# Kernel tuning notes

Measured on AMD Instinct MI355X. Metric: run time of the kernel, lower is better.

The kernel has to match this reference:

```python
import jax, jax.numpy as jnp
import numpy as np

LN_EPS = 1e-6


def setup_inputs() -> dict:
    key = jax.random.key(0)
    ks = jax.random.split(key, 8)
    B, C, E, S, K = 2, 32, 128, 64, 7  # E = exp_r * C
    x = jax.random.normal(ks[0], (B, C, S, S, S), jnp.float32)
    mask = (jax.random.uniform(ks[1], (B, 1, S, S, S)) < 0.3).astype(jnp.int32)
    w_dw = jax.random.normal(ks[2], (C, 1, K, K, K), jnp.float32) * 0.05  # depthwise, groups=C
    b_dw = jnp.zeros((C,), jnp.float32)
    ln_g = jnp.ones((C,), jnp.float32)
    ln_b = jnp.zeros((C,), jnp.float32)
    w2 = jax.random.normal(ks[3], (E, C), jnp.float32) * (1.0 / np.sqrt(C))  # 1x1 expand
    b2 = jnp.zeros((E,), jnp.float32)
    w3 = jax.random.normal(ks[4], (C, E), jnp.float32) * (1.0 / np.sqrt(E))  # 1x1 project
    b3 = jnp.zeros((C,), jnp.float32)
    return {"x": x, "mask": mask, "w_dw": w_dw, "b_dw": b_dw,
            "ln_g": ln_g, "ln_b": ln_b, "w2": w2, "b2": b2, "w3": w3, "b3": b3}


def reference(x, mask, w_dw, b_dw, ln_g, ln_b, w2, b2, w3, b3):
    m = mask.astype(x.dtype)                      # [B,1,D,H,W] active-site indicator
    cexp = lambda v: v[None, :, None, None, None]
    xm = x * m                                    # sparse tensor: zeros off the active set
    # submanifold depthwise conv: gather only active neighbors, emit only at active sites
    C = w_dw.shape[0]
    y = jax.lax.conv_general_dilated(
        xm, w_dw, window_strides=(1, 1, 1), padding='SAME',
        feature_group_count=C,
        dimension_numbers=('NCDHW', 'OIDHW', 'NCDHW'))
    y = (y + cexp(b_dw)) * m
    # ConvNeXt LayerNorm: per-voxel over channels, only on active sites
    mu = y.mean(axis=1, keepdims=True)
    var = ((y - mu) ** 2).mean(axis=1, keepdims=True)
    yn = ((y - mu) * jax.lax.rsqrt(var + LN_EPS) * cexp(ln_g) + cexp(ln_b)) * m
    # 1x1 expand + GELU (exact, matching nn.GELU default)
    h = jax.nn.gelu(jnp.einsum('bcdhw,ec->bedhw', yn, w2) + cexp(b2), approximate=False) * m
    # 1x1 project
    o = (jnp.einsum('bedhw,ce->bcdhw', h, w3) + cexp(b3)) * m
    # residual (do_res=True)
    return xm + o
```

## Files before the change

kernel.cpp:

```cpp
#include <hip/hip_runtime.h>

#define S 64
#define S2 4096
#define S3 262144
#define NVOX (2 * S3)
#define C 32
#define E 128
#define LN_EPS 1e-6f

#define ROWSLOT 40
#define NROWS  196
#define HALO_SZ (ROWSLOT * NROWS)

__device__ __forceinline__ unsigned f2b_bits(float f) {
    union { float f; unsigned u; } x; x.f = f;
    unsigned r = x.u + 0x7fffu + ((x.u >> 16) & 1u);
    return r >> 16;
}
__device__ __forceinline__ float hi2f(unsigned u) {
    union { unsigned u; float f; } x; x.u = u & 0xffff0000u; return x.f;
}
__device__ __forceinline__ float lo2f(unsigned u) {
    union { unsigned u; float f; } x; x.u = u << 16; return x.f;
}

__global__ __launch_bounds__(256) void k_conv(
    const float* __restrict__ x,
    const int* __restrict__ mask,
    const float* __restrict__ wdw,
    const float* __restrict__ bdw,
    float* __restrict__ y)
{
    __shared__ unsigned halo[HALO_SZ];

    const int bx = blockIdx.x;
    const int by = blockIdx.y;
    const int b  = by >> 5;
    const int c  = by & 31;
    const int d0 = (bx >> 3) * 8;
    const int h0 = (bx & 7) * 8;
    const int tid = threadIdx.x;

    const float* xc = x + (size_t)(b * C + c) * S3;
    const int* mb = mask + (size_t)b * S3;

    for (int t = tid; t < NROWS * 36; t += 256) {
        int r = t / 36;
        int j = t - r * 36;
        if (j < 35) {
            int Dk = r / 14;
            int m  = r - Dk * 14;
            int gh = h0 + m - 3;
            int gd = d0 + Dk - 3;
            unsigned lo = 0, hi = 0;
            if ((unsigned)gh < 64u && (unsigned)gd < 64u) {
                int rowoff = gd * S2 + gh * S;
                int gw0 = 2 * j - 3;
                int gw1 = gw0 + 1;
                if ((unsigned)gw0 < 64u) {
                    float xv = xc[rowoff + gw0];
                    int   mv = mb[rowoff + gw0];
                    lo = mv ? f2b_bits(xv) : 0u;
                }
                if ((unsigned)gw1 < 64u) {
                    float xv = xc[rowoff + gw1];
                    int   mv = mb[rowoff + gw1];
                    hi = mv ? f2b_bits(xv) : 0u;
                }
            }
            halo[ROWSLOT * r + ((m >> 1) & 3) + j] = lo | (hi << 16);
        }
    }
    __syncthreads();

    const int wq = tid & 7;
    const int hg = (tid >> 3) & 3;
    const int dd = tid >> 5;

    float acc0[8], acc1[8];
    #pragma unroll
    for (int j = 0; j < 8; ++j) { acc0[j] = 0.f; acc1[j] = 0.f; }

    const float* wc = wdw + c * 343;

    for (int kd = 0; kd < 7; ++kd) {
        const int Dk = dd + kd;
        #pragma unroll
        for (int t = 0; t < 8; ++t) {
            const int m  = 2 * hg + t;
            const int rb = ROWSLOT * (14 * Dk + m) + ((m >> 1) & 3) + 4 * wq;
            unsigned dw[7];
            #pragma unroll
            for (int p = 0; p < 7; ++p) dw[p] = halo[rb + p];
            float in14[14];
            #pragma unroll
            for (int p = 0; p < 7; ++p) {
                in14[2 * p]     = lo2f(dw[p]);
                in14[2 * p + 1] = hi2f(dw[p]);
            }
            if (t <= 6) {
                const float* wr = wc + kd * 49 + t * 7;
                #pragma unroll
                for (int kw = 0; kw < 7; ++kw) {
                    float wt = wr[kw];
                    #pragma unroll
                    for (int j = 0; j < 8; ++j)
                        acc0[j] = fmaf(wt, in14[j + kw], acc0[j]);
                }
            }
            if (t >= 1) {
                const float* wr = wc + kd * 49 + (t - 1) * 7;
                #pragma unroll
                for (int kw = 0; kw < 7; ++kw) {
                    float wt = wr[kw];
                    #pragma unroll
                    for (int j = 0; j < 8; ++j)
                        acc1[j] = fmaf(wt, in14[j + kw], acc1[j]);
                }
            }
        }
    }

    const int w0  = wq << 3;
    const int gd  = d0 + dd;
    const int gh0 = h0 + 2 * hg;
    const float bb = bdw[c];
    const size_t obase = (size_t)(b * C + c) * S3 + gd * S2 + gh0 * S + w0;
    const int mbase = gd * S2 + gh0 * S + w0;

    float ov[8];
    #pragma unroll
    for (int j = 0; j < 8; ++j)
        ov[j] = (mb[mbase + j] != 0) ? (acc0[j] + bb) : 0.f;
    *(float4*)(y + obase)     = make_float4(ov[0], ov[1], ov[2], ov[3]);
    *(float4*)(y + obase + 4) = make_float4(ov[4], ov[5], ov[6], ov[7]);

    #pragma unroll
    for (int j = 0; j < 8; ++j)
        ov[j] = (mb[mbase + S + j] != 0) ? (acc1[j] + bb) : 0.f;
    *(float4*)(y + obase + S)     = make_float4(ov[0], ov[1], ov[2], ov[3]);
    *(float4*)(y + obase + S + 4) = make_float4(ov[4], ov[5], ov[6], ov[7]);
}

__global__ __launch_bounds__(256) void k_count(
    const int* __restrict__ mask, int* __restrict__ bcnt)
{
    int v = blockIdx.x * 256 + threadIdx.x;
    int act = (mask[v] != 0) ? 1 : 0;
    unsigned long long ball = __ballot(act);
    __shared__ int wsum[4];
    int lane = threadIdx.x & 63, wid = threadIdx.x >> 6;
    if (lane == 0) wsum[wid] = __popcll(ball);
    __syncthreads();
    if (threadIdx.x == 0)
        bcnt[blockIdx.x] = wsum[0] + wsum[1] + wsum[2] + wsum[3];
}

__global__ __launch_bounds__(256) void k_scan(
    const int* __restrict__ bcnt, int* __restrict__ bbase, int* __restrict__ ntot)
{
    int t = threadIdx.x;
    int cv[8]; int s = 0;
    #pragma unroll
    for (int j = 0; j < 8; ++j) { cv[j] = bcnt[t * 8 + j]; s += cv[j]; }
    int lane = t & 63, wid = t >> 6;
    int x = s;
    #pragma unroll
    for (int off = 1; off < 64; off <<= 1) {
        int yv = __shfl_up(x, off, 64);
        if (lane >= off) x += yv;
    }
    __shared__ int wtot[4];
    if (lane == 63) wtot[wid] = x;
    __syncthreads();
    int wbase = 0;
    for (int w = 0; w < wid; ++w) wbase += wtot[w];
    int run = wbase + x - s;
    #pragma unroll
    for (int j = 0; j < 8; ++j) { bbase[t * 8 + j] = run; run += cv[j]; }
    if (t == 255) *ntot = run;
}

__global__ __launch_bounds__(256) void k_scatter(
    const int* __restrict__ mask, const int* __restrict__ bbase,
    int* __restrict__ list)
{
    int v = blockIdx.x * 256 + threadIdx.x;
    int act = (mask[v] != 0) ? 1 : 0;
    unsigned long long ball = __ballot(act);
    int lane = threadIdx.x & 63, wid = threadIdx.x >> 6;
    __shared__ int wcnt[4];
    if (lane == 0) wcnt[wid] = __popcll(ball);
    __syncthreads();
    int base = bbase[blockIdx.x];
    for (int w = 0; w < wid; ++w) base += wcnt[w];
    int pre = __popcll(ball & ((1ull << lane) - 1ull));
    if (act) list[base + pre] = v;
}

__device__ __forceinline__ float erf_fast(float z) {
    float az = fabsf(z);
    float t = __builtin_amdgcn_rcpf(fmaf(0.3275911f, az, 1.f));
    float p = t * fmaf(t, fmaf(t, fmaf(t, fmaf(t, 1.061405429f, -1.453152027f),
                     1.421413741f), -0.284496736f), 0.254829592f);
    float r = 1.f - p * __expf(-az * az);
    return copysignf(r, z);
}

__global__ __launch_bounds__(256) void k_mlp(
    const float* __restrict__ x,
    const float* __restrict__ lng,
    const float* __restrict__ lnb,
    const float* __restrict__ w2,
    const float* __restrict__ b2v,
    const float* __restrict__ w3,
    const float* __restrict__ b3v,
    const int* __restrict__ mask,
    const int* __restrict__ ntot,
    const int* __restrict__ list,
    float* __restrict__ out)
{
    int i = blockIdx.x * 256 + threadIdx.x;
    int v;
    if (list != nullptr) {
        if (i >= *ntot) return;
        v = list[i];
    } else {
        v = i;
        if (mask[v] == 0) return;
    }
    const int b = v >> 18;
    const int s = v & (S3 - 1);
    const size_t base = (size_t)b * C * S3 + s;

    float yv[32];
    #pragma unroll
    for (int c = 0; c < 32; ++c) yv[c] = out[base + (size_t)c * S3];

    float mu = 0.f;
    #pragma unroll
    for (int c = 0; c < 32; ++c) mu += yv[c];
    mu *= (1.f / 32.f);
    float var = 0.f;
    #pragma unroll
    for (int c = 0; c < 32; ++c) { float d = yv[c] - mu; var += d * d; }
    var *= (1.f / 32.f);
    const float rs = rsqrtf(var + LN_EPS);
    #pragma unroll
    for (int c = 0; c < 32; ++c)
        yv[c] = (yv[c] - mu) * rs * lng[c] + lnb[c];

    float o[32];
    #pragma unroll
    for (int c = 0; c < 32; ++c) o[c] = b3v[c];

    const float4* w3q = (const float4*)w3;
    for (int e0 = 0; e0 < E; e0 += 4) {
        float a0 = b2v[e0], a1 = b2v[e0 + 1], a2 = b2v[e0 + 2], a3 = b2v[e0 + 3];
        const float* w2r = w2 + e0 * 32;
        #pragma unroll
        for (int c = 0; c < 32; ++c) {
            float yc = yv[c];
            a0 = fmaf(w2r[c],      yc, a0);
            a1 = fmaf(w2r[32 + c], yc, a1);
            a2 = fmaf(w2r[64 + c], yc, a2);
            a3 = fmaf(w2r[96 + c], yc, a3);
        }
        const float k = 0.70710678118654752f;
        float g0 = 0.5f * a0 * (1.f + erf_fast(a0 * k));
        float g1 = 0.5f * a1 * (1.f + erf_fast(a1 * k));
        float g2 = 0.5f * a2 * (1.f + erf_fast(a2 * k));
        float g3 = 0.5f * a3 * (1.f + erf_fast(a3 * k));
        const int eq = e0 >> 2;
        #pragma unroll
        for (int c = 0; c < 32; ++c) {
            float4 wv = w3q[c * 32 + eq];
            float oc = o[c];
            oc = fmaf(wv.x, g0, oc);
            oc = fmaf(wv.y, g1, oc);
            oc = fmaf(wv.z, g2, oc);
            oc = fmaf(wv.w, g3, oc);
            o[c] = oc;
        }
    }

    #pragma unroll
    for (int c = 0; c < 32; ++c) {
        float xm = x[base + (size_t)c * S3];
        out[base + (size_t)c * S3] = xm + o[c];
    }
}

extern "C" void kernel_launch(void* const* d_in, const int* in_sizes, int n_in,
                              void* d_out, int out_size, void* d_ws, size_t ws_size,
                              hipStream_t stream)
{
    const float* x   = (const float*)d_in[0];
    const int*   m   = (const int*)d_in[1];
    const float* wdw = (const float*)d_in[2];
    const float* bdw = (const float*)d_in[3];
    const float* lng = (const float*)d_in[4];
    const float* lnb = (const float*)d_in[5];
    const float* w2  = (const float*)d_in[6];
    const float* b2v = (const float*)d_in[7];
    const float* w3  = (const float*)d_in[8];
    const float* b3v = (const float*)d_in[9];
    float* out = (float*)d_out;

    k_conv<<<dim3(64, 64), 256, 0, stream>>>(x, m, wdw, bdw, out);

    const size_t need = 256 + 8192 + 8192 + (size_t)NVOX * sizeof(int);
    if (ws_size >= need) {
        int* ntot  = (int*)d_ws;
        int* bcnt  = (int*)((char*)d_ws + 256);
        int* bbase = (int*)((char*)d_ws + 256 + 8192);
        int* list  = (int*)((char*)d_ws + 256 + 16384);
        k_count  <<<2048, 256, 0, stream>>>(m, bcnt);
        k_scan   <<<1,    256, 0, stream>>>(bcnt, bbase, ntot);
        k_scatter<<<2048, 256, 0, stream>>>(m, bbase, list);
        k_mlp<<<2048, 256, 0, stream>>>(x, lng, lnb, w2, b2v, w3, b3v,
                                        m, ntot, list, out);
    } else {
        k_mlp<<<2048, 256, 0, stream>>>(x, lng, lnb, w2, b2v, w3, b3v,
                                        m, nullptr, nullptr, out);
    }
}
```

Before: 465.0 us.

## Run depthwise 3D conv on bf16 MFMA with precomputed banded weight fragments

Replaces the VALU FMA depthwise convolution with a matrix-core version. A small pre-kernel expands each 7-tap weight row into a banded Toeplitz bf16 fragment. The conv kernel then issues 16x16x32 bf16 MFMAs over a larger halo tile (8x16 output rows per block, 512 threads). The aim is to move the 343-tap FMA work onto matrix units, at the cost of an extra kernel launch, extra workspace, and wasted MFMA lanes on the zero band entries. The old VALU path is kept as a fallback when the workspace is too small.

```diff
diff --git a/kernel.cpp b/kernel.cpp
--- a/kernel.cpp
+++ b/kernel.cpp
@@ -8,9 +8,8 @@
 #define E 128
 #define LN_EPS 1e-6f
 
-#define ROWSLOT 40
-#define NROWS  196
-#define HALO_SZ (ROWSLOT * NROWS)
+typedef short short8 __attribute__((ext_vector_type(8)));
+typedef float f32x4  __attribute__((ext_vector_type(4)));
 
 __device__ __forceinline__ unsigned f2b_bits(float f) {
     union { float f; unsigned u; } x; x.f = f;
@@ -24,15 +23,150 @@
     union { unsigned u; float f; } x; x.u = u << 16; return x.f;
 }
 
-__global__ __launch_bounds__(256) void k_conv(
+__global__ __launch_bounds__(64) void k_wfrag(
+    const float* __restrict__ wdw, unsigned* __restrict__ frag)
+{
+    const int kdkh = blockIdx.x;
+    const int c    = blockIdx.y;
+    const int L = threadIdx.x;
+    const int m = L & 15, q = L >> 4;
+    const float* w = wdw + c * 343 + kdkh * 7;
+    unsigned dwv[4];
+    #pragma unroll
+    for (int p = 0; p < 4; ++p) {
+        int kw0 = 8 * q + 2 * p - m;
+        int kw1 = kw0 + 1;
+        unsigned lo = ((unsigned)kw0 < 7u) ? f2b_bits(w[kw0]) : 0u;
+        unsigned hi = ((unsigned)kw1 < 7u) ? f2b_bits(w[kw1]) : 0u;
+        dwv[p] = lo | (hi << 16);
+    }
+    *(uint4*)(frag + (c * 49 + kdkh) * 256 + L * 4) =
+        make_uint4(dwv[0], dwv[1], dwv[2], dwv[3]);
+}
+
+#define HALO_DW 11088
+__global__ __launch_bounds__(512) void k_conv_mfma(
+    const float* __restrict__ x,
+    const int* __restrict__ mask,
+    const unsigned* __restrict__ frag,
+    const float* __restrict__ bdw,
+    float* __restrict__ y)
+{
+    __shared__ uint4 halo4[(HALO_DW + 4) / 4 + 1];
+    unsigned* halo = (unsigned*)halo4;
+
+    const int bx = blockIdx.x;
+    const int by = blockIdx.y;
+    const int b  = by >> 5;
+    const int c  = by & 31;
+    const int d0 = (bx >> 2) * 8;
+    const int h0 = (bx & 3) * 16;
+    const int tid = threadIdx.x;
+
+    const float* xc = x + (size_t)(b * C + c) * S3;
+    const int* mb = mask + (size_t)b * S3;
+
+    for (int t = tid; t < HALO_DW; t += 512) {
+        int r = t / 36;
+        int j = t - r * 36;
+        int Dk = r / 22;
+        int m  = r - Dk * 22;
+        int gd = d0 + Dk - 3, gh = h0 + m - 3;
+        unsigned lo = 0, hi = 0;
+        if ((unsigned)gd < 64u && (unsigned)gh < 64u) {
+            int ro = gd * S2 + gh * S;
+            int gw0 = 2 * j - 3;
+            int gw1 = gw0 + 1;
+            if ((unsigned)gw0 < 64u) {
+                float xv = xc[ro + gw0]; int mv = mb[ro + gw0];
+                lo = mv ? f2b_bits(xv) : 0u;
+            }
+            if ((unsigned)gw1 < 64u) {
+                float xv = xc[ro + gw1]; int mv = mb[ro + gw1];
+                hi = mv ? f2b_bits(xv) : 0u;
+            }
+        }
+        halo[t] = lo | (hi << 16);
+    }
+    if (tid < 8) halo[HALO_DW + tid] = 0;
+    __syncthreads();
+
+    const int lane = tid & 63;
+    const int n = lane & 15, q = lane >> 4;
+    const int wv = tid >> 6;
+    const int dd0 = (wv >> 1) * 2;
+    const int w0a = (wv & 1) * 32, w0b = w0a + 16;
+
+    f32x4 aA0 = {0,0,0,0}, aA1 = {0,0,0,0};
+    f32x4 aB0 = {0,0,0,0}, aB1 = {0,0,0,0};
+
+    const unsigned* fb = frag + (c * 49) * 256 + (lane << 2);
+
+    for (int kh = 0; kh < 7; ++kh) {
+        short8 wf[7];
+        #pragma unroll
+        for (int k = 0; k < 7; ++k)
+            wf[k] = *(const short8*)(fb + ((k * 7 + kh) << 8));
+        #pragma unroll
+        for (int i = 0; i < 8; ++i) {
+            const int Dk = dd0 + i;
+            const int rdw = (Dk * 22 + n + kh) * 36 + (q << 2);
+            short8 b0 = *(const short8*)&halo4[(rdw + (w0a >> 1)) >> 2];
+            short8 b1 = *(const short8*)&halo4[(rdw + (w0b >> 1)) >> 2];
+            if (i <= 6) {
+                aA0 = __builtin_amdgcn_mfma_f32_16x16x32_bf16(wf[i], b0, aA0, 0, 0, 0);
+                aA1 = __builtin_amdgcn_mfma_f32_16x16x32_bf16(wf[i], b1, aA1, 0, 0, 0);
+            }
+            if (i >= 1) {
+                aB0 = __builtin_amdgcn_mfma_f32_16x16x32_bf16(wf[i-1], b0, aB0, 0, 0, 0);
+                aB1 = __builtin_amdgcn_mfma_f32_16x16x32_bf16(wf[i-1], b1, aB1, 0, 0, 0);
+            }
+        }
+    }
+
+    const float bb = bdw[c];
+    const int gh = h0 + n;
+    #pragma unroll
+    for (int s = 0; s < 2; ++s) {
+        const int gd = d0 + dd0 + s;
+        const size_t ob = (size_t)(b * C + c) * S3 + gd * S2 + gh * S;
+        const int mo = gd * S2 + gh * S;
+        f32x4 a0 = s == 0 ? aA0 : aB0;
+        f32x4 a1 = s == 0 ? aA1 : aB1;
+        {
+            int wq = w0a + (q << 2);
+            int4 mv = *(const int4*)(mb + mo + wq);
+            float4 o;
+            o.x = mv.x ? a0[0] + bb : 0.f;
+            o.y = mv.y ? a0[1] + bb : 0.f;
+            o.z = mv.z ? a0[2] + bb : 0.f;
+            o.w = mv.w ? a0[3] + bb : 0.f;
+            *(float4*)(y + ob + wq) = o;
+        }
+        {
+            int wq = w0b + (q << 2);
+            int4 mv = *(const int4*)(mb + mo + wq);
+            float4 o;
+            o.x = mv.x ? a1[0] + bb : 0.f;
+            o.y = mv.y ? a1[1] + bb : 0.f;
+            o.z = mv.z ? a1[2] + bb : 0.f;
+            o.w = mv.w ? a1[3] + bb : 0.f;
+            *(float4*)(y + ob + wq) = o;
+        }
+    }
+}
+
+#define VROWSLOT 40
+#define VNROWS  196
+#define VHALO_SZ (VROWSLOT * VNROWS)
+__global__ __launch_bounds__(256) void k_conv_valu(
     const float* __restrict__ x,
     const int* __restrict__ mask,
     const float* __restrict__ wdw,
     const float* __restrict__ bdw,
     float* __restrict__ y)
 {
-    __shared__ unsigned halo[HALO_SZ];
-
+    __shared__ unsigned halo[VHALO_SZ];
     const int bx = blockIdx.x;
     const int by = blockIdx.y;
     const int b  = by >> 5;
@@ -40,11 +174,10 @@
     const int d0 = (bx >> 3) * 8;
     const int h0 = (bx & 7) * 8;
     const int tid = threadIdx.x;
-
     const float* xc = x + (size_t)(b * C + c) * S3;
     const int* mb = mask + (size_t)b * S3;
 
-    for (int t = tid; t < NROWS * 36; t += 256) {
+    for (int t = tid; t < VNROWS * 36; t += 256) {
         int r = t / 36;
         int j = t - r * 36;
         if (j < 35) {
@@ -55,20 +188,17 @@
             unsigned lo = 0, hi = 0;
             if ((unsigned)gh < 64u && (unsigned)gd < 64u) {
                 int rowoff = gd * S2 + gh * S;
-                int gw0 = 2 * j - 3;
-                int gw1 = gw0 + 1;
+                int gw0 = 2 * j - 3, gw1 = gw0 + 1;
                 if ((unsigned)gw0 < 64u) {
-                    float xv = xc[rowoff + gw0];
-                    int   mv = mb[rowoff + gw0];
+                    float xv = xc[rowoff + gw0]; int mv = mb[rowoff + gw0];
                     lo = mv ? f2b_bits(xv) : 0u;
                 }
                 if ((unsigned)gw1 < 64u) {
-                    float xv = xc[rowoff + gw1];
-                    int   mv = mb[rowoff + gw1];
+                    float xv = xc[rowoff + gw1]; int mv = mb[rowoff + gw1];
                     hi = mv ? f2b_bits(xv) : 0u;
                 }
             }
-            halo[ROWSLOT * r + ((m >> 1) & 3) + j] = lo | (hi << 16);
+            halo[VROWSLOT * r + ((m >> 1) & 3) + j] = lo | (hi << 16);
         }
     }
     __syncthreads();
@@ -76,11 +206,9 @@
     const int wq = tid & 7;
     const int hg = (tid >> 3) & 3;
     const int dd = tid >> 5;
-
     float acc0[8], acc1[8];
     #pragma unroll
     for (int j = 0; j < 8; ++j) { acc0[j] = 0.f; acc1[j] = 0.f; }
-
     const float* wc = wdw + c * 343;
 
     for (int kd = 0; kd < 7; ++kd) {
@@ -88,7 +216,7 @@
         #pragma unroll
         for (int t = 0; t < 8; ++t) {
             const int m  = 2 * hg + t;
-            const int rb = ROWSLOT * (14 * Dk + m) + ((m >> 1) & 3) + 4 * wq;
+            const int rb = VROWSLOT * (14 * Dk + m) + ((m >> 1) & 3) + 4 * wq;
             unsigned dw[7];
             #pragma unroll
             for (int p = 0; p < 7; ++p) dw[p] = halo[rb + p];
@@ -127,14 +255,12 @@
     const float bb = bdw[c];
     const size_t obase = (size_t)(b * C + c) * S3 + gd * S2 + gh0 * S + w0;
     const int mbase = gd * S2 + gh0 * S + w0;
-
     float ov[8];
     #pragma unroll
     for (int j = 0; j < 8; ++j)
         ov[j] = (mb[mbase + j] != 0) ? (acc0[j] + bb) : 0.f;
     *(float4*)(y + obase)     = make_float4(ov[0], ov[1], ov[2], ov[3]);
     *(float4*)(y + obase + 4) = make_float4(ov[4], ov[5], ov[6], ov[7]);
-
     #pragma unroll
     for (int j = 0; j < 8; ++j)
         ov[j] = (mb[mbase + S + j] != 0) ? (acc1[j] + bb) : 0.f;
@@ -307,14 +433,25 @@
     const float* b3v = (const float*)d_in[9];
     float* out = (float*)d_out;
 
-    k_conv<<<dim3(64, 64), 256, 0, stream>>>(x, m, wdw, bdw, out);
-
-    const size_t need = 256 + 8192 + 8192 + (size_t)NVOX * sizeof(int);
-    if (ws_size >= need) {
+    const size_t off_list = 256 + 8192 + 8192;
+    const size_t off_frag = off_list + (size_t)NVOX * sizeof(int);
+    const size_t frag_sz  = (size_t)32 * 49 * 1024;
+    const size_t need_mfma    = off_frag + frag_sz;
+    const size_t need_compact = off_frag;
+
+    if (ws_size >= need_mfma) {
+        unsigned* fragbuf = (unsigned*)((char*)d_ws + off_frag);
+        k_wfrag<<<dim3(49, 32), 64, 0, stream>>>(wdw, fragbuf);
+        k_conv_mfma<<<dim3(32, 64), 512, 0, stream>>>(x, m, fragbuf, bdw, out);
+    } else {
+        k_conv_valu<<<dim3(64, 64), 256, 0, stream>>>(x, m, wdw, bdw, out);
+    }
+
+    if (ws_size >= need_compact) {
         int* ntot  = (int*)d_ws;
         int* bcnt  = (int*)((char*)d_ws + 256);
         int* bbase = (int*)((char*)d_ws + 256 + 8192);
-        int* list  = (int*)((char*)d_ws + 256 + 16384);
+        int* list  = (int*)((char*)d_ws + off_list);
         k_count  <<<2048, 256, 0, stream>>>(m, bcnt);
         k_scan   <<<1,    256, 0, stream>>>(bcnt, bbase, ntot);
         k_scatter<<<2048, 256, 0, stream>>>(m, bbase, list);
```

Measured after the change: 389.7 us. -16.2%, faster.
